# Performance work log

Hardware: AMD Instinct MI355X
Metric: run time of the kernel (lower is better)

Reference implementation:

```python
import jax, jax.numpy as jnp
import numpy as np
from jax import lax

EPS = 1e-5
HEADS = 4
NPOINT = 512


def _layernorm(x, g, b):
    mu = jnp.mean(x, axis=-1, keepdims=True)
    var = jnp.var(x, axis=-1, keepdims=True)
    return (x - mu) * lax.rsqrt(var + EPS) * g + b


def farthest_point_sample(xyz, npoint):
    # xyz: [B, N, 3] -> idx [B, npoint]  (canonical PointNet++ FPS, seeded at point 0)
    B, N, _ = xyz.shape

    def step(carry, _):
        dist, far = carry  # [B,N], [B]
        centroid = jnp.take_along_axis(xyz, far[:, None, None], axis=1)  # [B,1,3]
        d = jnp.sum((xyz - centroid) ** 2, axis=-1)  # [B,N]
        dist = jnp.minimum(dist, d)
        nxt = jnp.argmax(dist, axis=1).astype(jnp.int32)
        return (dist, nxt), far

    init = (jnp.full((B, N), 1e10, xyz.dtype), jnp.zeros((B,), jnp.int32))
    _, idx = lax.scan(step, init, None, length=npoint)  # [npoint, B]
    return idx.T  # [B, npoint]


def index_points(points, idx):
    # points: [B, N, D], idx: [B, S] -> [B, S, D]
    return jnp.take_along_axis(points, idx[..., None], axis=1)


def setup_inputs() -> dict:
    key = jax.random.key(0)
    ks = iter(jax.random.split(key, 16))
    B, N, Cin, D, Dff, Dout = 8, 2048, 64, 128, 512, 256
    w = lambda k, s: (jax.random.normal(k, s, jnp.float32) * 0.02)
    inp = {
        "xyz": jax.random.normal(next(ks), (B, 3, N), jnp.float32),
        "points": jax.random.normal(next(ks), (B, Cin, N), jnp.float32),
        "W_proj": w(next(ks), (D, Cin)), "b_proj": jnp.zeros((D,)),
        "bn1_g": jnp.ones((D,)), "bn1_b": jnp.zeros((D,)),
        "bn1_m": jnp.zeros((D,)), "bn1_v": jnp.ones((D,)),
        "W_pos": w(next(ks), (D, 3)), "b_pos": jnp.zeros((D,)),
        "Wq": w(next(ks), (D, D)), "bq": jnp.zeros((D,)),
        "Wk": w(next(ks), (D, D)), "bk": jnp.zeros((D,)),
        "Wv": w(next(ks), (D, D)), "bv": jnp.zeros((D,)),
        "Wo": w(next(ks), (D, D)), "bo": jnp.zeros((D,)),
        "ln1_g": jnp.ones((D,)), "ln1_b": jnp.zeros((D,)),
        "W1": w(next(ks), (Dff, D)), "b1": jnp.zeros((Dff,)),
        "W2": w(next(ks), (D, Dff)), "b2": jnp.zeros((D,)),
        "ln2_g": jnp.ones((D,)), "ln2_b": jnp.zeros((D,)),
        "W_fc": w(next(ks), (Dout, D + 3)), "b_fc": jnp.zeros((Dout,)),
        "bn2_g": jnp.ones((Dout,)), "bn2_b": jnp.zeros((Dout,)),
        "bn2_m": jnp.zeros((Dout,)), "bn2_v": jnp.ones((Dout,)),
    }
    return inp


def reference(xyz, points, W_proj, b_proj, bn1_g, bn1_b, bn1_m, bn1_v,
              W_pos, b_pos, Wq, bq, Wk, bk, Wv, bv, Wo, bo,
              ln1_g, ln1_b, W1, b1, W2, b2, ln2_g, ln2_b,
              W_fc, b_fc, bn2_g, bn2_b, bn2_m, bn2_v):
    B, _, N = xyz.shape
    D = W_proj.shape[0]
    hd = D // HEADS

    # project: pointwise conv + BN (inference), output [B, N, D]
    feat = jnp.einsum('dc,bcn->bnd', W_proj, points) + b_proj
    feat = (feat - bn1_m) * lax.rsqrt(bn1_v + EPS) * bn1_g + bn1_b

    # transformer block with xyz positional encoding
    pos = jnp.einsum('dc,bcn->bnd', W_pos, xyz) + b_pos
    x = feat + pos
    q = (x @ Wq.T + bq).reshape(B, N, HEADS, hd)
    k = (x @ Wk.T + bk).reshape(B, N, HEADS, hd)
    v = (x @ Wv.T + bv).reshape(B, N, HEADS, hd)
    scores = jnp.einsum('bnhd,bmhd->bhnm', q, k) / jnp.sqrt(jnp.float32(hd))
    attn = jax.nn.softmax(scores, axis=-1)
    o = jnp.einsum('bhnm,bmhd->bnhd', attn, v).reshape(B, N, D)
    x = _layernorm(x + (o @ Wo.T + bo), ln1_g, ln1_b)
    ffn = jax.nn.relu(x @ W1.T + b1) @ W2.T + b2
    features = _layernorm(x + ffn, ln2_g, ln2_b)  # [B, N, D]

    # sampling + gather
    xyz_t = jnp.transpose(xyz, (0, 2, 1))  # [B, N, 3]
    fps_idx = farthest_point_sample(xyz_t, NPOINT)  # [B, npoint]
    new_points = index_points(features, fps_idx)    # [B, npoint, D]
    new_xyz = index_points(xyz_t, fps_idx)          # [B, npoint, 3]

    cat = jnp.concatenate([new_points, new_xyz], axis=-1)  # [B, npoint, D+3]
    out = jnp.einsum('od,bnd->bon', W_fc, cat) + b_fc[None, :, None]
    out = (out - bn2_m[None, :, None]) * lax.rsqrt(bn2_v + EPS)[None, :, None] \
          * bn2_g[None, :, None] + bn2_b[None, :, None]
    out = jax.nn.relu(out)  # [B, Dout, npoint]

    return jnp.transpose(new_xyz, (0, 2, 1)), out
```

## Files before the change

kernel.cpp:

```cpp
#include <hip/hip_runtime.h>
#include <hip/hip_bf16.h>

#define B_    8
#define N_    2048
#define CIN_  64
#define D_    128
#define DFF_  512
#define DOUT_ 256
#define S_    512
#define H_    4
#define HD_   32
#define EPS_  1e-5f

typedef unsigned short u16;
typedef unsigned long long u64;
typedef __attribute__((ext_vector_type(8))) short short8v;
typedef __attribute__((ext_vector_type(4))) float f32x4;

__device__ __forceinline__ u16 f2bu(float f) {
  __hip_bfloat16 h = __float2bfloat16(f);
  return *(u16*)&h;
}
__device__ __forceinline__ float bu2f(u16 u) {
  __hip_bfloat16 h = *(__hip_bfloat16*)&u;
  return __bfloat162float(h);
}

#define OW_QKV 0
#define OW_O   49152
#define OW_1   65536
#define OW_2   131072
#define OW_FC  196608
#define OW_CAT 237568
#define NW_TOT 249856

__global__ __launch_bounds__(256) void prep_kernel(
    const float* __restrict__ Wq, const float* __restrict__ bq,
    const float* __restrict__ Wk, const float* __restrict__ bk,
    const float* __restrict__ Wv, const float* __restrict__ bv,
    const float* __restrict__ Wo, const float* __restrict__ W1,
    const float* __restrict__ W2, const float* __restrict__ Wfc,
    const float* __restrict__ bfc, const float* __restrict__ Wp,
    const float* __restrict__ bp, const float* __restrict__ Wpos,
    const float* __restrict__ bpos, const float* __restrict__ g1,
    const float* __restrict__ be1, const float* __restrict__ m1,
    const float* __restrict__ v1, const float* __restrict__ g2,
    const float* __restrict__ bb2, const float* __restrict__ m2,
    const float* __restrict__ v2, u16* __restrict__ wb,
    float* __restrict__ fb) {
  const float SC = 0.1767766952966369f * 1.4426950408889634f;
  int i = blockIdx.x * 256 + threadIdx.x;
  if (i < OW_O) {
    int n = i >> 7, k = i & 127;
    float v = (n < 128) ? Wq[i] * SC
                        : (n < 256) ? Wk[(n - 128) * 128 + k]
                                    : Wv[(n - 256) * 128 + k];
    wb[OW_QKV + i] = f2bu(v);
  } else if (i < OW_1) {
    wb[i] = f2bu(Wo[i - OW_O]);
  } else if (i < OW_2) {
    wb[i] = f2bu(W1[i - OW_1]);
  } else if (i < OW_FC) {
    wb[i] = f2bu(W2[i - OW_2]);
  } else if (i < OW_CAT) {
    int j = i - OW_FC;
    int n = j / 160, c = j % 160;
    wb[i] = f2bu(c < 131 ? Wfc[n * 131 + c] : 0.f);
  } else if (i < NW_TOT) {
    int j = i - OW_CAT;
    int d = j / 96, c = j % 96;
    float v;
    if (c < 64) v = Wp[d * 64 + c] * (g1[d] * rsqrtf(v1[d] + EPS_));
    else if (c < 67) v = Wpos[d * 3 + (c - 64)];
    else v = 0.f;
    wb[i] = f2bu(v);
  } else if (i < NW_TOT + 384) {
    int n = i - NW_TOT;
    fb[n] = (n < 128) ? bq[n] * SC : (n < 256) ? bk[n - 128] : bv[n - 256];
  } else if (i < NW_TOT + 512) {
    int d = i - (NW_TOT + 384);
    float s1 = g1[d] * rsqrtf(v1[d] + EPS_);
    fb[384 + d] = (bp[d] - m1[d]) * s1 + be1[d] + bpos[d];
  } else if (i < NW_TOT + 768) {
    int n = i - (NW_TOT + 512);
    fb[512 + n] = g2[n] * rsqrtf(v2[n] + EPS_);
  } else if (i < NW_TOT + 1024) {
    int n = i - (NW_TOT + 768);
    float s = g2[n] * rsqrtf(v2[n] + EPS_);
    fb[768 + n] = bfc[n] * s + bb2[n] - m2[n] * s;
  }
}

#define FPS_SMEM 320

template <int CTRL, int RM>
__device__ __forceinline__ float dppmax(float v) {
  int m = __builtin_amdgcn_update_dpp(__float_as_int(v), __float_as_int(v),
                                      CTRL, RM, 0xF, true);
  return fmaxf(v, __int_as_float(m));
}

__device__ __forceinline__ void fps_slice(
    char* smem, int b, const float* __restrict__ xyz,
    float* __restrict__ dist_ws, int* __restrict__ far_ws,
    int* __restrict__ idx_out, float* __restrict__ out0, int s0, int s1) {
  u64* keys = (u64*)smem;
  float* crd = (float*)(smem + 64);
  const int t = threadIdx.x, w = t >> 6, lane = t & 63;
  const float* xb = xyz + (size_t)b * 3 * N_;
  const int base = (w * 64 + lane) * 8;
  float* dw = dist_ws + b * N_;
  float px[8], py[8], pz[8], dist[8];
#pragma unroll
  for (int j = 0; j < 8; j++) {
    px[j] = xb[base + j];
    py[j] = xb[N_ + base + j];
    pz[j] = xb[2 * N_ + base + j];
    dist[j] = 1e10f;
  }
  if (s0 != 0) {
#pragma unroll
    for (int j = 0; j < 8; j++) dist[j] = dw[base + j];
  }
  int far = (s0 == 0) ? 0 : far_ws[b];
  float cx = xb[far], cy = xb[N_ + far], cz = xb[2 * N_ + far];
  for (int s = s0; s < s1; s++) {
    if (t == 0) {
      idx_out[b * S_ + s] = far;
      out0[(size_t)b * 3 * S_ + s] = cx;
      out0[(size_t)b * 3 * S_ + S_ + s] = cy;
      out0[(size_t)b * 3 * S_ + 2 * S_ + s] = cz;
    }
    float best = -1.0f, bx = 0.f, by = 0.f, bz = 0.f;
    int bestp = 0;
#pragma unroll
    for (int j = 0; j < 8; j++) {
      float dx = __fsub_rn(px[j], cx);
      float dy = __fsub_rn(py[j], cy);
      float dz = __fsub_rn(pz[j], cz);
      float d = __fadd_rn(__fadd_rn(__fmul_rn(dx, dx), __fmul_rn(dy, dy)),
                          __fmul_rn(dz, dz));
      float nd = fminf(dist[j], d);
      dist[j] = nd;
      if (nd > best) {
        best = nd; bestp = base + j;
        bx = px[j]; by = py[j]; bz = pz[j];
      }
    }
    float m = best;
    m = dppmax<0x111, 0xF>(m);
    m = dppmax<0x112, 0xF>(m);
    m = dppmax<0x114, 0xF>(m);
    m = dppmax<0x118, 0xF>(m);
    m = dppmax<0x142, 0xA>(m);
    m = dppmax<0x143, 0xC>(m);
    float M = __int_as_float(__builtin_amdgcn_readlane(__float_as_int(m), 63));
    u64 mask = __ballot(best == M);
    int wl = __ffsll((long long)mask) - 1;
    if (lane == wl) {
      int sb = (s & 1) * 4 + w;
      keys[sb] = ((u64)__float_as_uint(M) << 32) |
                 (unsigned)(0xFFFFFFFFu - (unsigned)bestp);
      crd[sb * 3 + 0] = bx;
      crd[sb * 3 + 1] = by;
      crd[sb * 3 + 2] = bz;
    }
    asm volatile("s_waitcnt lgkmcnt(0)" ::: "memory");
    __builtin_amdgcn_s_barrier();
    asm volatile("" ::: "memory");
    const int q0 = (s & 1) * 4;
    u64 kk = keys[q0];
    float ccx = crd[q0 * 3], ccy = crd[q0 * 3 + 1], ccz = crd[q0 * 3 + 2];
#pragma unroll
    for (int i = 1; i < 4; i++) {
      u64 ki = keys[q0 + i];
      bool c = ki > kk;
      kk = c ? ki : kk;
      ccx = c ? crd[(q0 + i) * 3] : ccx;
      ccy = c ? crd[(q0 + i) * 3 + 1] : ccy;
      ccz = c ? crd[(q0 + i) * 3 + 2] : ccz;
    }
    far = (int)(0xFFFFFFFFu - (unsigned)kk);
    cx = ccx; cy = ccy; cz = ccz;
  }
#pragma unroll
  for (int j = 0; j < 8; j++) dw[base + j] = dist[j];
  if (t == 0) far_ws[b] = far;
}

template <int K, int KC, int ASTAGE, int EPI>
__global__ __launch_bounds__(256) void gemm_k(
    const u16* __restrict__ A, const u16* __restrict__ W,
    const float* __restrict__ srcf0, const float* __restrict__ srcf1,
    const int* __restrict__ fidx, const float* __restrict__ p0,
    const float* __restrict__ p1, const float* __restrict__ p2,
    const u16* __restrict__ resid, u16* __restrict__ outb,
    float* __restrict__ outf, int ntn, int fpsnb, int s0, int s1,
    const float* fxyz, float* fdist, int* ffar, int* fidxo, float* fout0) {
  constexpr int KP = KC + 8;
  constexpr int GEMM_SMEM = 2 * 128 * KP * 2;
  constexpr int SMEM = GEMM_SMEM > FPS_SMEM ? GEMM_SMEM : FPS_SMEM;
  __shared__ __align__(16) char smem[SMEM];
  if ((int)blockIdx.x < fpsnb) {
    fps_slice(smem, blockIdx.x, fxyz, fdist, ffar, fidxo, fout0, s0, s1);
    return;
  }
  u16 (*As)[KP] = (u16 (*)[KP])smem;
  u16 (*Ws)[KP] = (u16 (*)[KP])(smem + 128 * KP * 2);
  const int bid = blockIdx.x - fpsnb;
  const int mt = bid / ntn, nt = bid % ntn;
  const int t = threadIdx.x, w = t >> 6, lane = t & 63;
  const int g = lane >> 4, lr = lane & 15;

  f32x4 acc[2][8];
#pragma unroll
  for (int qf = 0; qf < 2; qf++)
#pragma unroll
    for (int nf = 0; nf < 8; nf++) acc[qf][nf] = {0.f, 0.f, 0.f, 0.f};

  for (int kc = 0; kc < K / KC; kc++) {
    __syncthreads();
    for (int i = t; i < 128 * (KC / 8); i += 256) {
      int row = i / (KC / 8), c8 = i % (KC / 8);
      *(short8v*)&Ws[row][c8 * 8] =
          *(const short8v*)(W + (size_t)(nt * 128 + row) * K + kc * KC + c8 * 8);
    }
    if constexpr (ASTAGE == 0) {
      for (int i = t; i < 128 * (KC / 8); i += 256) {
        int row = i / (KC / 8), c8 = i % (KC / 8);
        *(short8v*)&As[row][c8 * 8] =
            *(const short8v*)(A + (size_t)(mt * 128 + row) * K + kc * KC + c8 * 8);
      }
    } else if constexpr (ASTAGE == 1) {
      int bb = (mt * 128) >> 11, n0 = (mt * 128) & (N_ - 1);
      for (int i = t; i < 96 * 128; i += 256) {
        int c = i >> 7, n = i & 127;
        float v;
        if (c < 64) v = srcf0[((size_t)bb * CIN_ + c) * N_ + n0 + n];
        else if (c < 67) v = srcf1[((size_t)bb * 3 + (c - 64)) * N_ + n0 + n];
        else v = 0.f;
        As[n][c] = f2bu(v);
      }
    } else {
      int bb = (mt * 128) >> 9, sq0 = (mt * 128) & (S_ - 1);
      for (int i = t; i < 128 * 20; i += 256) {
        int row = i / 20, c8 = i % 20;
        int id = fidx[bb * S_ + sq0 + row];
        short8v val;
        if (c8 < 16) {
          val = *(const short8v*)(A + ((size_t)bb * N_ + id) * D_ + c8 * 8);
        } else if (c8 == 16) {
          val = short8v{0, 0, 0, 0, 0, 0, 0, 0};
          val[0] = (short)f2bu(srcf1[((size_t)bb * 3 + 0) * N_ + id]);
          val[1] = (short)f2bu(srcf1[((size_t)bb * 3 + 1) * N_ + id]);
          val[2] = (short)f2bu(srcf1[((size_t)bb * 3 + 2) * N_ + id]);
        } else {
          val = short8v{0, 0, 0, 0, 0, 0, 0, 0};
        }
        *(short8v*)&As[row][c8 * 8] = val;
      }
    }
    __syncthreads();
#pragma unroll
    for (int ks = 0; ks < KC / 32; ks++) {
      short8v a0 = *(const short8v*)&As[w * 32 + lr][ks * 32 + 8 * g];
      short8v a1 = *(const short8v*)&As[w * 32 + 16 + lr][ks * 32 + 8 * g];
#pragma unroll
      for (int nf = 0; nf < 8; nf++) {
        short8v bb = *(const short8v*)&Ws[nf * 16 + lr][ks * 32 + 8 * g];
        acc[0][nf] = __builtin_amdgcn_mfma_f32_16x16x32_bf16(a0, bb, acc[0][nf], 0, 0, 0);
        acc[1][nf] = __builtin_amdgcn_mfma_f32_16x16x32_bf16(a1, bb, acc[1][nf], 0, 0, 0);
      }
    }
  }

  if constexpr (EPI == 3) {
#pragma unroll
    for (int qf = 0; qf < 2; qf++) {
#pragma unroll
      for (int i = 0; i < 4; i++) {
        int m = mt * 128 + w * 32 + qf * 16 + 4 * g + i;
        float v[8], sm = 0.f, sq = 0.f;
#pragma unroll
        for (int nf = 0; nf < 8; nf++) {
          int n = nf * 16 + lr;
          float x = acc[qf][nf][i] + p0[n] + bu2f(resid[(size_t)m * D_ + n]);
          v[nf] = x;
          sm += x;
          sq += x * x;
        }
#pragma unroll
        for (int msk = 1; msk < 16; msk <<= 1) {
          sm += __shfl_xor(sm, msk);
          sq += __shfl_xor(sq, msk);
        }
        float mu = sm * (1.f / 128.f);
        float var = sq * (1.f / 128.f) - mu * mu;
        float rs = rsqrtf(var + EPS_);
#pragma unroll
        for (int nf = 0; nf < 8; nf++) {
          int n = nf * 16 + lr;
          outb[(size_t)m * D_ + n] = f2bu((v[nf] - mu) * rs * p1[n] + p2[n]);
        }
      }
    }
  } else if constexpr (EPI == 1) {
    if (nt < 2) {
#pragma unroll
      for (int qf = 0; qf < 2; qf++)
#pragma unroll
        for (int nf = 0; nf < 8; nf++)
#pragma unroll
          for (int i = 0; i < 4; i++) {
            int m = mt * 128 + w * 32 + qf * 16 + 4 * g + i;
            int n = nt * 128 + nf * 16 + lr;
            float vv = acc[qf][nf][i] + p0[n];
            int hh = (n >> 5) & 3, c = n & 31;
            int bb = m >> 11, tok = m & (N_ - 1);
            outb[(size_t)nt * 2097152 +
                 (((size_t)bb * H_ + hh) * N_ + tok) * HD_ + c] = f2bu(vv);
          }
    } else {
      __syncthreads();
      u16 (*Vt)[KP] = (u16 (*)[KP])smem;
#pragma unroll
      for (int qf = 0; qf < 2; qf++)
#pragma unroll
        for (int nf = 0; nf < 8; nf++)
#pragma unroll
          for (int i = 0; i < 4; i++) {
            int m_l = w * 32 + qf * 16 + 4 * g + i;
            int n_l = nf * 16 + lr;
            Vt[n_l][m_l] = f2bu(acc[qf][nf][i] + p0[256 + n_l]);
          }
      __syncthreads();
      int bb = (mt * 128) >> 11, tok0 = (mt * 128) & (N_ - 1);
      for (int i2 = t; i2 < 2048; i2 += 256) {
        int row = i2 >> 4, seg = i2 & 15;
        *(short8v*)(outb + (size_t)2 * 2097152 +
                    (((size_t)bb * H_ + (row >> 5)) * HD_ + (row & 31)) * N_ +
                    tok0 + seg * 8) = *(const short8v*)&Vt[row][seg * 8];
      }
    }
  } else {
#pragma unroll
    for (int qf = 0; qf < 2; qf++)
#pragma unroll
      for (int nf = 0; nf < 8; nf++)
#pragma unroll
        for (int i = 0; i < 4; i++) {
          int m = mt * 128 + w * 32 + qf * 16 + 4 * g + i;
          int nl = nf * 16 + lr;
          int n = nt * 128 + nl;
          float vv = acc[qf][nf][i];
          if constexpr (EPI == 0) {
            outb[(size_t)m * D_ + nl] = f2bu(vv + p0[n]);
          } else if constexpr (EPI == 2) {
            outb[(size_t)m * DFF_ + n] = f2bu(fmaxf(vv + p0[n], 0.f));
          } else {
            float r = fmaxf(vv * p1[n] + p2[n], 0.f);
            outf[((size_t)(m >> 9) * DOUT_ + n) * S_ + (m & (S_ - 1))] = r;
          }
        }
  }
}

__global__ __launch_bounds__(256) void attn_mfma_kernel(
    const u16* __restrict__ qg, const u16* __restrict__ kg,
    const u16* __restrict__ vg, u16* __restrict__ o, int fpsnb, int s0, int s1,
    const float* fxyz, float* fdist, int* ffar, int* fidxo, float* fout0) {
  constexpr int ATTN_SMEM = 64 * 40 * 2 + 32 * 72 * 2 + 4 * 16 * 72 * 2;
  constexpr int SMEM = ATTN_SMEM > FPS_SMEM ? ATTN_SMEM : FPS_SMEM;
  __shared__ __align__(16) char smem[SMEM];
  if ((int)blockIdx.x < fpsnb) {
    fps_slice(smem, blockIdx.x, fxyz, fdist, ffar, fidxo, fout0, s0, s1);
    return;
  }
  const int t = threadIdx.x;
  const int w = t >> 6, lane = t & 63, g = lane >> 4, lr = lane & 15;
  u16 (*ks)[40] = (u16 (*)[40])smem;
  u16 (*vt)[72] = (u16 (*)[72])(smem + 5120);
  u16 (*psw)[72] = (u16 (*)[72])(smem + 9728) + w * 16;

  const int bid = blockIdx.x - fpsnb;
  const int qt = bid & 31;
  const int bh = bid >> 5;
  const int b = bh >> 2, h = bh & 3;
  const int qrow = qt * 64 + w * 16 + lr;

  short8v aq = *(const short8v*)(qg + ((size_t)bh * N_ + qrow) * HD_ + 8 * g);

  const u16* kb = kg + (size_t)bh * N_ * HD_;
  const u16* vbt = vg + (size_t)bh * N_ * HD_;

  const f32x4 fzero = {0.f, 0.f, 0.f, 0.f};
  float mrun = -INFINITY, lrun = 0.f;
  f32x4 acco[2] = {fzero, fzero};

  const int krow = t >> 2, kseg = (t & 3) * 8;
  const int vrow = t >> 3, vseg = (t & 7) * 8;

  for (int ch = 0; ch < 32; ch++) {
    __syncthreads();
    *(short8v*)(&ks[krow][kseg]) =
        *(const short8v*)(kb + (size_t)(ch * 64 + krow) * HD_ + kseg);
    *(short8v*)(&vt[vrow][vseg]) =
        *(const short8v*)(vbt + (size_t)vrow * N_ + ch * 64 + vseg);
    __syncthreads();

    f32x4 stv[4];
#pragma unroll
    for (int kt = 0; kt < 4; kt++) {
      short8v ak = *(const short8v*)(&ks[kt * 16 + lr][8 * g]);
      stv[kt] = __builtin_amdgcn_mfma_f32_16x16x32_bf16(ak, aq, fzero, 0, 0, 0);
    }

    float mx = -INFINITY;
#pragma unroll
    for (int kt = 0; kt < 4; kt++)
#pragma unroll
      for (int i = 0; i < 4; i++) mx = fmaxf(mx, stv[kt][i]);
    mx = fmaxf(mx, __shfl_xor(mx, 16));
    mx = fmaxf(mx, __shfl_xor(mx, 32));
    float nm = fmaxf(mrun, mx);
    float alpha = exp2f(mrun - nm);
    mrun = nm;
    float psum = 0.f;
#pragma unroll
    for (int kt = 0; kt < 4; kt++) {
      float p0 = exp2f(stv[kt][0] - nm);
      float p1 = exp2f(stv[kt][1] - nm);
      float p2 = exp2f(stv[kt][2] - nm);
      float p3 = exp2f(stv[kt][3] - nm);
      psum += (p0 + p1) + (p2 + p3);
      u64 pk = (u64)f2bu(p0) | ((u64)f2bu(p1) << 16) |
               ((u64)f2bu(p2) << 32) | ((u64)f2bu(p3) << 48);
      *(u64*)(&psw[lr][kt * 16 + 4 * g]) = pk;
    }
    psum += __shfl_xor(psum, 16);
    psum += __shfl_xor(psum, 32);
    lrun = lrun * alpha + psum;
#pragma unroll
    for (int dt = 0; dt < 2; dt++)
#pragma unroll
      for (int i = 0; i < 4; i++) acco[dt][i] *= alpha;

#pragma unroll
    for (int mc = 0; mc < 2; mc++) {
      short8v pb = *(const short8v*)(&psw[lr][mc * 32 + 8 * g]);
#pragma unroll
      for (int dt = 0; dt < 2; dt++) {
        short8v av = *(const short8v*)(&vt[dt * 16 + lr][mc * 32 + 8 * g]);
        acco[dt] = __builtin_amdgcn_mfma_f32_16x16x32_bf16(av, pb, acco[dt], 0, 0, 0);
      }
    }
  }

  float rl = 1.0f / lrun;
#pragma unroll
  for (int dt = 0; dt < 2; dt++) {
    u64 pk = (u64)f2bu(acco[dt][0] * rl) | ((u64)f2bu(acco[dt][1] * rl) << 16) |
             ((u64)f2bu(acco[dt][2] * rl) << 32) |
             ((u64)f2bu(acco[dt][3] * rl) << 48);
    *(u64*)(o + ((size_t)b * N_ + qrow) * D_ + h * HD_ + dt * 16 + 4 * g) = pk;
  }
}

extern "C" void kernel_launch(void* const* d_in, const int* in_sizes, int n_in,
                              void* d_out, int out_size, void* d_ws, size_t ws_size,
                              hipStream_t stream) {
  const float* xyz    = (const float*)d_in[0];
  const float* points = (const float*)d_in[1];
  const float* Wp     = (const float*)d_in[2];
  const float* bp     = (const float*)d_in[3];
  const float* g1     = (const float*)d_in[4];
  const float* be1    = (const float*)d_in[5];
  const float* m1     = (const float*)d_in[6];
  const float* v1     = (const float*)d_in[7];
  const float* Wpos   = (const float*)d_in[8];
  const float* bpos   = (const float*)d_in[9];
  const float* Wq     = (const float*)d_in[10];
  const float* bq     = (const float*)d_in[11];
  const float* Wk     = (const float*)d_in[12];
  const float* bk     = (const float*)d_in[13];
  const float* Wv     = (const float*)d_in[14];
  const float* bv     = (const float*)d_in[15];
  const float* Wo     = (const float*)d_in[16];
  const float* bo     = (const float*)d_in[17];
  const float* lg1    = (const float*)d_in[18];
  const float* lb1    = (const float*)d_in[19];
  const float* W1     = (const float*)d_in[20];
  const float* b1     = (const float*)d_in[21];
  const float* W2     = (const float*)d_in[22];
  const float* b2p    = (const float*)d_in[23];
  const float* lg2    = (const float*)d_in[24];
  const float* lb2    = (const float*)d_in[25];
  const float* Wfc    = (const float*)d_in[26];
  const float* bfc    = (const float*)d_in[27];
  const float* g2     = (const float*)d_in[28];
  const float* bb2    = (const float*)d_in[29];
  const float* m2     = (const float*)d_in[30];
  const float* v2     = (const float*)d_in[31];

  float* out0 = (float*)d_out;
  float* out1 = out0 + (size_t)B_ * 3 * S_;

  char* ws = (char*)d_ws;
  int*   fps_idx = (int*)ws;
  u16*   wb      = (u16*)(ws + 16384);
  float* fb      = (float*)(ws + 516096);
  float* dist_ws = (float*)(ws + 520192);
  int*   far_ws  = (int*)(ws + 585728);
  const size_t MB = 1024 * 1024;
  u16* x     = (u16*)(ws + 1 * MB);
  u16* o     = (u16*)(ws + 5 * MB);
  u16* x2    = (u16*)(ws + 9 * MB);
  u16* feats = (u16*)(ws + 13 * MB);
  u16* qb    = (u16*)(ws + 17 * MB);
  u16* h     = (u16*)(ws + 29 * MB);

  prep_kernel<<<980, 256, 0, stream>>>(Wq, bq, Wk, bk, Wv, bv, Wo, W1, W2, Wfc,
                                       bfc, Wp, bp, Wpos, bpos, g1, be1, m1, v1,
                                       g2, bb2, m2, v2, wb, fb);

  gemm_k<96, 96, 1, 0><<<8 + 128, 256, 0, stream>>>(
      nullptr, wb + OW_CAT, points, xyz, nullptr, fb + 384, nullptr, nullptr,
      nullptr, x, nullptr, 1, 8, 0, 64, xyz, dist_ws, far_ws, fps_idx, out0);
  gemm_k<128, 128, 0, 1><<<8 + 384, 256, 0, stream>>>(
      x, wb + OW_QKV, nullptr, nullptr, nullptr, fb, nullptr, nullptr,
      nullptr, qb, nullptr, 3, 8, 64, 156, xyz, dist_ws, far_ws, fps_idx, out0);
  attn_mfma_kernel<<<8 + B_ * H_ * (N_ / 64), 256, 0, stream>>>(
      qb, qb + 2097152, qb + 2 * 2097152, o, 8, 156, 264, xyz, dist_ws, far_ws,
      fps_idx, out0);
  gemm_k<128, 128, 0, 3><<<8 + 128, 256, 0, stream>>>(
      o, wb + OW_O, nullptr, nullptr, nullptr, bo, lg1, lb1, x, x2, nullptr, 1,
      8, 264, 336, xyz, dist_ws, far_ws, fps_idx, out0);
  gemm_k<128, 128, 0, 2><<<8 + 512, 256, 0, stream>>>(
      x2, wb + OW_1, nullptr, nullptr, nullptr, b1, nullptr, nullptr,
      nullptr, h, nullptr, 4, 8, 336, 440, xyz, dist_ws, far_ws, fps_idx, out0);
  gemm_k<512, 128, 0, 3><<<8 + 128, 256, 0, stream>>>(
      h, wb + OW_2, nullptr, nullptr, nullptr, b2p, lg2, lb2, x2, feats,
      nullptr, 1, 8, 440, 512, xyz, dist_ws, far_ws, fps_idx, out0);
  gemm_k<160, 160, 2, 4><<<64, 256, 0, stream>>>(
      feats, wb + OW_FC, nullptr, xyz, fps_idx, nullptr, fb + 512, fb + 768,
      nullptr, nullptr, out1, 2, 0, 0, 0, nullptr, nullptr, nullptr, nullptr,
      nullptr);
}
```

Measured before the change: 385.1 us.

## Fold softmax row sums into MFMA, add lazy rescale, tree-reduce FPS keys

The attention kernel appends a ones row to the V tile so the PV MFMA also produces the softmax denominator. This removes the per-chunk psum shuffles. The running max is only updated and the accumulators rescaled when the new max exceeds the old one by more than 8, and probabilities are packed to bf16 with v_cvt_pk_bf16_f32. The FPS cross-wave argmax becomes a pairwise tree that uses vector LDS loads, and the FPS step split across fused kernels is rebalanced toward the attention kernel. This costs one extra MFMA column tile and more LDS, and lazy rescaling risks precision loss in bf16 if exponents grow up to 2^8.

```diff
diff --git a/kernel.cpp b/kernel.cpp
--- a/kernel.cpp
+++ b/kernel.cpp
@@ -13,6 +13,7 @@
 #define EPS_  1e-5f
 
 typedef unsigned short u16;
+typedef unsigned int u32;
 typedef unsigned long long u64;
 typedef __attribute__((ext_vector_type(8))) short short8v;
 typedef __attribute__((ext_vector_type(4))) float f32x4;
@@ -169,19 +170,21 @@
     __builtin_amdgcn_s_barrier();
     asm volatile("" ::: "memory");
     const int q0 = (s & 1) * 4;
-    u64 kk = keys[q0];
-    float ccx = crd[q0 * 3], ccy = crd[q0 * 3 + 1], ccz = crd[q0 * 3 + 2];
-#pragma unroll
-    for (int i = 1; i < 4; i++) {
-      u64 ki = keys[q0 + i];
-      bool c = ki > kk;
-      kk = c ? ki : kk;
-      ccx = c ? crd[(q0 + i) * 3] : ccx;
-      ccy = c ? crd[(q0 + i) * 3 + 1] : ccy;
-      ccz = c ? crd[(q0 + i) * 3 + 2] : ccz;
-    }
+    u64 k0 = keys[q0], k1 = keys[q0 + 1], k2 = keys[q0 + 2], k3 = keys[q0 + 3];
+    const f32x4* crd4 = (const f32x4*)(crd + q0 * 3);
+    f32x4 v0 = crd4[0], v1 = crd4[1], v2 = crd4[2];
+    bool c01 = k0 >= k1;
+    u64 ka = c01 ? k0 : k1;
+    float xa = c01 ? v0[0] : v0[3], ya = c01 ? v0[1] : v1[0],
+          za = c01 ? v0[2] : v1[1];
+    bool c23 = k2 >= k3;
+    u64 kb = c23 ? k2 : k3;
+    float xv = c23 ? v1[2] : v2[1], yv = c23 ? v1[3] : v2[2],
+          zv = c23 ? v2[0] : v2[3];
+    bool cf = ka >= kb;
+    u64 kk = cf ? ka : kb;
+    cx = cf ? xa : xv; cy = cf ? ya : yv; cz = cf ? za : zv;
     far = (int)(0xFFFFFFFFu - (unsigned)kk);
-    cx = ccx; cy = ccy; cz = ccz;
   }
 #pragma unroll
   for (int j = 0; j < 8; j++) dw[base + j] = dist[j];
@@ -369,7 +372,7 @@
     const u16* __restrict__ qg, const u16* __restrict__ kg,
     const u16* __restrict__ vg, u16* __restrict__ o, int fpsnb, int s0, int s1,
     const float* fxyz, float* fdist, int* ffar, int* fidxo, float* fout0) {
-  constexpr int ATTN_SMEM = 64 * 40 * 2 + 32 * 72 * 2 + 4 * 16 * 72 * 2;
+  constexpr int ATTN_SMEM = 64 * 40 * 2 + 48 * 72 * 2 + 4 * 16 * 72 * 2;
   constexpr int SMEM = ATTN_SMEM > FPS_SMEM ? ATTN_SMEM : FPS_SMEM;
   __shared__ __align__(16) char smem[SMEM];
   if ((int)blockIdx.x < fpsnb) {
@@ -380,7 +383,7 @@
   const int w = t >> 6, lane = t & 63, g = lane >> 4, lr = lane & 15;
   u16 (*ks)[40] = (u16 (*)[40])smem;
   u16 (*vt)[72] = (u16 (*)[72])(smem + 5120);
-  u16 (*psw)[72] = (u16 (*)[72])(smem + 9728) + w * 16;
+  u16 (*psw)[72] = (u16 (*)[72])(smem + 12032) + w * 16;
 
   const int bid = blockIdx.x - fpsnb;
   const int qt = bid & 31;
@@ -388,14 +391,19 @@
   const int b = bh >> 2, h = bh & 3;
   const int qrow = qt * 64 + w * 16 + lr;
 
+  for (int i = t; i < 16 * 72; i += 256) {
+    int r = i / 72, c = i % 72;
+    vt[32 + r][c] = (r == 0) ? (u16)0x3F80 : (u16)0;
+  }
+
   short8v aq = *(const short8v*)(qg + ((size_t)bh * N_ + qrow) * HD_ + 8 * g);
 
   const u16* kb = kg + (size_t)bh * N_ * HD_;
   const u16* vbt = vg + (size_t)bh * N_ * HD_;
 
   const f32x4 fzero = {0.f, 0.f, 0.f, 0.f};
-  float mrun = -INFINITY, lrun = 0.f;
-  f32x4 acco[2] = {fzero, fzero};
+  float mrun = -INFINITY;
+  f32x4 acco[3] = {fzero, fzero, fzero};
 
   const int krow = t >> 2, kseg = (t & 3) * 8;
   const int vrow = t >> 3, vseg = (t & 7) * 8;
@@ -422,41 +430,41 @@
       for (int i = 0; i < 4; i++) mx = fmaxf(mx, stv[kt][i]);
     mx = fmaxf(mx, __shfl_xor(mx, 16));
     mx = fmaxf(mx, __shfl_xor(mx, 32));
-    float nm = fmaxf(mrun, mx);
-    float alpha = exp2f(mrun - nm);
-    mrun = nm;
-    float psum = 0.f;
+    if (!__all(mx - mrun <= 8.0f)) {
+      float nm = fmaxf(mrun, mx);
+      float alpha = exp2f(mrun - nm);
+      mrun = nm;
+#pragma unroll
+      for (int dt = 0; dt < 3; dt++)
+#pragma unroll
+        for (int i = 0; i < 4; i++) acco[dt][i] *= alpha;
+    }
 #pragma unroll
     for (int kt = 0; kt < 4; kt++) {
-      float p0 = exp2f(stv[kt][0] - nm);
-      float p1 = exp2f(stv[kt][1] - nm);
-      float p2 = exp2f(stv[kt][2] - nm);
-      float p3 = exp2f(stv[kt][3] - nm);
-      psum += (p0 + p1) + (p2 + p3);
-      u64 pk = (u64)f2bu(p0) | ((u64)f2bu(p1) << 16) |
-               ((u64)f2bu(p2) << 32) | ((u64)f2bu(p3) << 48);
+      float p0 = exp2f(stv[kt][0] - mrun);
+      float p1 = exp2f(stv[kt][1] - mrun);
+      float p2 = exp2f(stv[kt][2] - mrun);
+      float p3 = exp2f(stv[kt][3] - mrun);
+      u32 r01, r23;
+      asm("v_cvt_pk_bf16_f32 %0, %1, %2" : "=v"(r01) : "v"(p0), "v"(p1));
+      asm("v_cvt_pk_bf16_f32 %0, %1, %2" : "=v"(r23) : "v"(p2), "v"(p3));
+      u64 pk = (u64)r01 | ((u64)r23 << 32);
       *(u64*)(&psw[lr][kt * 16 + 4 * g]) = pk;
     }
-    psum += __shfl_xor(psum, 16);
-    psum += __shfl_xor(psum, 32);
-    lrun = lrun * alpha + psum;
-#pragma unroll
-    for (int dt = 0; dt < 2; dt++)
-#pragma unroll
-      for (int i = 0; i < 4; i++) acco[dt][i] *= alpha;
 
 #pragma unroll
     for (int mc = 0; mc < 2; mc++) {
       short8v pb = *(const short8v*)(&psw[lr][mc * 32 + 8 * g]);
 #pragma unroll
-      for (int dt = 0; dt < 2; dt++) {
+      for (int dt = 0; dt < 3; dt++) {
         short8v av = *(const short8v*)(&vt[dt * 16 + lr][mc * 32 + 8 * g]);
         acco[dt] = __builtin_amdgcn_mfma_f32_16x16x32_bf16(av, pb, acco[dt], 0, 0, 0);
       }
     }
   }
 
-  float rl = 1.0f / lrun;
+  float lsum = __shfl(acco[2][0], lr);
+  float rl = 1.0f / lsum;
 #pragma unroll
   for (int dt = 0; dt < 2; dt++) {
     u64 pk = (u64)f2bu(acco[dt][0] * rl) | ((u64)f2bu(acco[dt][1] * rl) << 16) |
@@ -528,16 +536,16 @@
       nullptr, x, nullptr, 1, 8, 0, 64, xyz, dist_ws, far_ws, fps_idx, out0);
   gemm_k<128, 128, 0, 1><<<8 + 384, 256, 0, stream>>>(
       x, wb + OW_QKV, nullptr, nullptr, nullptr, fb, nullptr, nullptr,
-      nullptr, qb, nullptr, 3, 8, 64, 156, xyz, dist_ws, far_ws, fps_idx, out0);
+      nullptr, qb, nullptr, 3, 8, 64, 160, xyz, dist_ws, far_ws, fps_idx, out0);
   attn_mfma_kernel<<<8 + B_ * H_ * (N_ / 64), 256, 0, stream>>>(
-      qb, qb + 2097152, qb + 2 * 2097152, o, 8, 156, 264, xyz, dist_ws, far_ws,
+      qb, qb + 2097152, qb + 2 * 2097152, o, 8, 160, 272, xyz, dist_ws, far_ws,
       fps_idx, out0);
   gemm_k<128, 128, 0, 3><<<8 + 128, 256, 0, stream>>>(
       o, wb + OW_O, nullptr, nullptr, nullptr, bo, lg1, lb1, x, x2, nullptr, 1,
-      8, 264, 336, xyz, dist_ws, far_ws, fps_idx, out0);
+      8, 272, 344, xyz, dist_ws, far_ws, fps_idx, out0);
   gemm_k<128, 128, 0, 2><<<8 + 512, 256, 0, stream>>>(
       x2, wb + OW_1, nullptr, nullptr, nullptr, b1, nullptr, nullptr,
-      nullptr, h, nullptr, 4, 8, 336, 440, xyz, dist_ws, far_ws, fps_idx, out0);
+      nullptr, h, nullptr, 4, 8, 344, 440, xyz, dist_ws, far_ws, fps_idx, out0);
   gemm_k<512, 128, 0, 3><<<8 + 128, 256, 0, stream>>>(
       h, wb + OW_2, nullptr, nullptr, nullptr, b2p, lg2, lb2, x2, feats,
       nullptr, 1, 8, 440, 512, xyz, dist_ws, far_ws, fps_idx, out0);
```

New measurement: 348.4 us. -9.5%, faster.
